# Performance work log

Hardware: AMD Instinct MI355X
Metric: run time of the kernel (lower is better)

## Reference

```python
import jax, jax.numpy as jnp
import numpy as np

B, T, DIM, H, BUCKET = 4, 4096, 1024, 16, 64
E = DIM // H          # head dim = 64
U = T // BUCKET       # number of buckets = 64
EPS = 1e-6


def setup_inputs() -> dict:
    key = jax.random.key(0)
    ks = jax.random.split(key, 5)
    scale = 1.0 / np.sqrt(DIM)
    return {
        "x": jax.random.normal(ks[0], (B, T, DIM), dtype=jnp.float32),
        "Wq": jax.random.normal(ks[1], (DIM, DIM), dtype=jnp.float32) * scale,
        "Wk": jax.random.normal(ks[2], (DIM, DIM), dtype=jnp.float32) * scale,
        "Wv": jax.random.normal(ks[3], (DIM, DIM), dtype=jnp.float32) * scale,
        "Wo": jax.random.normal(ks[4], (DIM, DIM), dtype=jnp.float32) * scale,
        "bo": jnp.zeros((DIM,), dtype=jnp.float32),
    }


def _causal_linear_attn(q, k, v):
    # q, k, v: [b, h, t, e]; psi(k) = elu(k) + 1; q softmaxed over feature dim
    q = jax.nn.softmax(q, axis=-1)
    k = jax.nn.elu(k) + 1.0
    bucket = lambda x: x.reshape(*x.shape[:-2], U, BUCKET, E)  # [b,h,u,n,e]
    b_q, b_k, b_v = bucket(q), bucket(k), bucket(v)
    # cumulative key sums per bucket: [b,h,u,d]
    b_k_cumsum = jnp.cumsum(b_k.sum(axis=-2), axis=2)
    # per-bucket context then cumulative over buckets: [b,h,u,d,e]
    context = jnp.einsum("bhund,bhune->bhude", b_k, b_v)
    context = jnp.cumsum(context, axis=2)
    context = context / (b_k_cumsum[..., None] + EPS)
    # shift by one bucket (blindspot): bucket u sees context through bucket u-1
    context = jnp.concatenate(
        [jnp.zeros_like(context[:, :, :1]), context[:, :, :-1]], axis=2
    )
    attn = jnp.einsum("bhund,bhude->bhune", b_q, context)
    return attn.reshape(q.shape)  # [b,h,t,e]


def reference(x, Wq, Wk, Wv, Wo, bo):
    b, t, _ = x.shape
    q = x @ Wq
    k = x @ Wk
    v = x @ Wv
    merge = lambda z: z.reshape(b, t, H, E).transpose(0, 2, 1, 3)  # [b,h,t,e]
    attn = _causal_linear_attn(merge(q), merge(k), merge(v))
    out = attn.transpose(0, 2, 1, 3).reshape(b, t, DIM)
    return out @ Wo + bo
```

## Files before the change

### kernel.cpp

```cpp
#include <hip/hip_runtime.h>


#define T_LEN 4096
#define DIMN  1024
#define NHEAD 16
#define NB    4
#define MROWS (NB * T_LEN)

typedef float f32x4 __attribute__((ext_vector_type(4)));
typedef short s16x8 __attribute__((ext_vector_type(8)));
typedef short s16x4 __attribute__((ext_vector_type(4)));
using u16 = unsigned short;

__device__ __forceinline__ u16 f2bf(float f) {
  unsigned int u = __float_as_uint(f);
  u += 0x7fffu + ((u >> 16) & 1u);
  return (u16)(u >> 16);
}
__device__ __forceinline__ float bf2f(u16 h) {
  return __uint_as_float(((unsigned int)h) << 16);
}
__device__ __forceinline__ int swz16k(int off) {
  return off ^ (((off >> 7) & 3) << 4);
}

__global__ __launch_bounds__(256) void cvt_all_kern(const float* __restrict__ x,
                                                    const float* __restrict__ W0,
                                                    const float* __restrict__ W1,
                                                    const float* __restrict__ W2,
                                                    const float* __restrict__ W3,
                                                    u16* __restrict__ WT,
                                                    u16* __restrict__ xb) {
  __shared__ float tile[64][65];
  const int tid = threadIdx.x;
  if (blockIdx.x < 1024) {
    const int blk = blockIdx.x & 255;
    const int sel = blockIdx.x >> 8;
    const float* W = (sel == 0) ? W0 : (sel == 1) ? W1 : (sel == 2) ? W2 : W3;
    u16* dst = WT + (size_t)sel * DIMN * DIMN;
    const int k0 = (blk >> 4) << 6;
    const int n0 = (blk & 15) << 6;
    const int r = tid >> 6;
    const int c = tid & 63;
#pragma unroll
    for (int i = 0; i < 16; ++i) {
      int row = (i << 2) + r;
      tile[row][c] = W[(size_t)(k0 + row) * DIMN + n0 + c];
    }
    __syncthreads();
#pragma unroll
    for (int i = 0; i < 16; ++i) {
      int row = (i << 2) + r;
      dst[(size_t)(n0 + row) * DIMN + k0 + c] = f2bf(tile[c][row]);
    }
  } else {
    size_t i = ((size_t)(blockIdx.x - 1024) * 256 + tid) * 4;
    f32x4 v = *(const f32x4*)(x + i);
    s16x4 o;
    o.x = (short)f2bf(v.x); o.y = (short)f2bf(v.y);
    o.z = (short)f2bf(v.z); o.w = (short)f2bf(v.w);
    *(s16x4*)(xb + i) = o;
  }
}

template <int MODE>
__global__ __launch_bounds__(512, 2) void gemm256(
    const u16* __restrict__ A, const u16* __restrict__ Bt,
    u16* __restrict__ dq, u16* __restrict__ dk, u16* __restrict__ dv,
    float* __restrict__ dO, const float* __restrict__ bias) {
  constexpr int K = 1024;
  constexpr int BNT = (MODE == 0) ? 12 : 4;
  constexpr int NT = K / 64;
  extern __shared__ char lds[];

  const int tid = threadIdx.x;
  const int l = tid & 63;
  const int w = tid >> 6;
  const int wm = w >> 2;
  const int wn = w & 3;

  const int xcd = (int)blockIdx.x & 7;
  const int idx = (int)blockIdx.x >> 3;
  const int g = idx / (4 * BNT);
  const int r2 = idx % (4 * BNT);
  const int bn = r2 >> 2;
  const int bm = xcd * 8 + g * 4 + (r2 & 3);
  const size_t arow0 = (size_t)bm * 256;
  const size_t brow0 = (size_t)bn * 256;

  int lrow[2], lcol[2];
#pragma unroll
  for (int i = 0; i < 2; ++i) {
    int lg = swz16k(tid * 16 + i * 8192);
    lrow[i] = lg >> 6;
    lcol[i] = (lg & 63) >> 1;
  }

  const int fr = l & 15;
  const int kswz = (((l >> 4) << 4)) ^ ((((fr >> 1) & 3)) << 4);

  auto STAGE = [&](int matsel, int kh, int tt) {
    const int kbase = (tt & (NT - 1)) * 64 + kh * 32;
#pragma unroll
    for (int i = 0; i < 2; ++i) {
      const u16* src = (matsel == 0)
          ? A  + (arow0 + (size_t)lrow[i]) * K + kbase + lcol[i]
          : Bt + (brow0 + (size_t)lrow[i]) * K + kbase + lcol[i];
      char* dst = lds + ((tt & 1) * 65536 + (matsel * 2 + kh) * 16384 +
                         i * 8192 + w * 1024);
      __builtin_amdgcn_global_load_lds(
          (__attribute__((address_space(1))) const void*)src,
          (__attribute__((address_space(3))) void*)dst, 16, 0, 0);
    }
  };
  auto LDA = [&](int buf, int kh, int rowb) -> s16x8 {
    return *(const s16x8*)(lds + buf * 65536 + kh * 16384 + rowb * 64 + kswz);
  };
  auto LDB = [&](int buf, int kh, int rowb) -> s16x8 {
    return *(const s16x8*)(lds + buf * 65536 + 32768 + kh * 16384 + rowb * 64 + kswz);
  };

  f32x4 acc[8][4];
#pragma unroll
  for (int i = 0; i < 8; ++i)
#pragma unroll
    for (int j = 0; j < 4; ++j) acc[i][j] = {0.f, 0.f, 0.f, 0.f};

  STAGE(0, 0, 0); STAGE(1, 0, 0); STAGE(0, 1, 0); STAGE(1, 1, 0);
  STAGE(0, 0, 1); STAGE(1, 0, 1);
  asm volatile("s_waitcnt vmcnt(8)" ::: "memory");
  __builtin_amdgcn_sched_barrier(0);
  __builtin_amdgcn_s_barrier();

  const int amb = wm * 128;
  const int bnb = wn * 64;
  s16x8 afA[4], afB[4], bfA[4], bfB[4];

#pragma unroll
  for (int i = 0; i < 4; ++i) afA[i] = LDA(0, 0, amb + i * 16 + fr);
#pragma unroll
  for (int i = 0; i < 4; ++i) bfA[i] = LDB(0, 0, bnb + i * 16 + fr);

#define MFMA_BLK(ACCOFF, AF, BF)                                              \
  __builtin_amdgcn_s_setprio(1);                                              \
  _Pragma("unroll")                                                           \
  for (int mi = 0; mi < 4; ++mi)                                              \
    _Pragma("unroll")                                                         \
    for (int ni = 0; ni < 4; ++ni)                                            \
      acc[(ACCOFF) + mi][ni] = __builtin_amdgcn_mfma_f32_16x16x32_bf16(       \
          AF[mi], BF[ni], acc[(ACCOFF) + mi][ni], 0, 0, 0);                   \
  __builtin_amdgcn_s_setprio(0);

#define PHASES(BUF, T)                                                        \
  {                                                                           \
    const int buf = (BUF);                                                    \
    const int t = (T);                                                        \
     \
    STAGE(0, 1, t + 1);                                                       \
    _Pragma("unroll")                                                         \
    for (int i = 0; i < 4; ++i) afB[i] = LDA(buf, 0, amb + (4 + i) * 16 + fr);\
    MFMA_BLK(0, afA, bfA)                                                     \
    __builtin_amdgcn_s_barrier();                                             \
      \
    STAGE(1, 1, t + 1);                                                       \
    asm volatile("s_waitcnt vmcnt(8)" ::: "memory");                          \
    __builtin_amdgcn_sched_barrier(0);                                        \
    _Pragma("unroll")                                                         \
    for (int i = 0; i < 4; ++i) afA[i] = LDA(buf, 1, amb + i * 16 + fr);      \
    _Pragma("unroll")                                                         \
    for (int i = 0; i < 4; ++i) bfB[i] = LDB(buf, 1, bnb + i * 16 + fr);      \
    MFMA_BLK(4, afB, bfA)                                                     \
    __builtin_amdgcn_s_barrier();                                             \
     \
    STAGE(0, 0, t + 2);                                                       \
    _Pragma("unroll")                                                         \
    for (int i = 0; i < 4; ++i) afB[i] = LDA(buf, 1, amb + (4 + i) * 16 + fr);\
    MFMA_BLK(0, afA, bfB)                                                     \
    __builtin_amdgcn_s_barrier();                                             \
       \
    STAGE(1, 0, t + 2);                                                       \
    asm volatile("s_waitcnt vmcnt(8)" ::: "memory");                          \
    __builtin_amdgcn_sched_barrier(0);                                        \
    _Pragma("unroll")                                                         \
    for (int i = 0; i < 4; ++i) afA[i] = LDA(buf ^ 1, 0, amb + i * 16 + fr);  \
    _Pragma("unroll")                                                         \
    for (int i = 0; i < 4; ++i) bfA[i] = LDB(buf ^ 1, 0, bnb + i * 16 + fr);  \
    MFMA_BLK(4, afB, bfB)                                                     \
    __builtin_amdgcn_s_barrier();                                             \
  }

#pragma unroll 1
  for (int th = 0; th < NT / 2; ++th) {
    PHASES(0, 2 * th)
    PHASES(1, 2 * th + 1)
  }
#undef PHASES
#undef MFMA_BLK

  const int r0 = (l >> 4) << 2;
  const int c0 = l & 15;
  if constexpr (MODE == 0) {
    const int mat = bn >> 2;
    u16* dst = (mat == 0) ? dq : ((mat == 1) ? dk : dv);
    const size_t colbase = (size_t)(bn & 3) * 256 + (size_t)wn * 64;
    if (mat == 0) {
#pragma unroll
      for (int mi = 0; mi < 8; ++mi) {
#pragma unroll
        for (int j = 0; j < 4; ++j) {
          float v0 = acc[mi][0][j], v1 = acc[mi][1][j];
          float v2 = acc[mi][2][j], v3 = acc[mi][3][j];
          float m = fmaxf(fmaxf(v0, v1), fmaxf(v2, v3));
#pragma unroll
          for (int off = 1; off < 16; off <<= 1) m = fmaxf(m, __shfl_xor(m, off));
          float e0 = __expf(v0 - m), e1 = __expf(v1 - m);
          float e2 = __expf(v2 - m), e3 = __expf(v3 - m);
          float s = e0 + e1 + e2 + e3;
#pragma unroll
          for (int off = 1; off < 16; off <<= 1) s += __shfl_xor(s, off);
          float inv = 1.f / s;
          const size_t row = arow0 + wm * 128 + mi * 16 + r0 + j;
          u16* p = dst + row * DIMN + colbase + c0;
          p[0]  = f2bf(e0 * inv); p[16] = f2bf(e1 * inv);
          p[32] = f2bf(e2 * inv); p[48] = f2bf(e3 * inv);
        }
      }
    } else {
#pragma unroll
      for (int mi = 0; mi < 8; ++mi)
#pragma unroll
        for (int ni = 0; ni < 4; ++ni)
#pragma unroll
          for (int j = 0; j < 4; ++j) {
            const size_t row = arow0 + wm * 128 + mi * 16 + r0 + j;
            float v = acc[mi][ni][j];
            float r = (mat == 1) ? (v > 0.f ? v + 1.f : __expf(v)) : v;
            dst[row * DIMN + colbase + ni * 16 + c0] = f2bf(r);
          }
    }
  } else {
    asm volatile("s_waitcnt vmcnt(0)" ::: "memory");
    __builtin_amdgcn_sched_barrier(0);
    __builtin_amdgcn_s_barrier();
    float* lf = (float*)lds;
#pragma unroll
    for (int half = 0; half < 2; ++half) {
      if (wm == half) {
#pragma unroll
        for (int mi = 0; mi < 8; ++mi)
#pragma unroll
          for (int ni = 0; ni < 4; ++ni) {
            const int col = wn * 64 + ni * 16 + c0;
            const float bv = bias[brow0 + col];
#pragma unroll
            for (int j = 0; j < 4; ++j) {
              const int row = mi * 16 + r0 + j;
              lf[row * 256 + (col ^ (((row >> 2) & 1) << 4))] =
                  acc[mi][ni][j] + bv;
            }
          }
      }
      __builtin_amdgcn_s_barrier();
#pragma unroll
      for (int i = 0; i < 16; ++i) {
        const int cid = tid + i * 512;
        const int r = cid >> 6;
        const int g2 = (cid & 63) * 4;
        const int pc = g2 ^ (((r >> 2) & 1) << 4);
        f32x4 vv = *(const f32x4*)&lf[r * 256 + pc];
        *(f32x4*)&dO[(arow0 + half * 128 + r) * DIMN + brow0 + g2] = vv;
      }
      __builtin_amdgcn_s_barrier();
    }
  }
}

__global__ __launch_bounds__(256) void ctx_bucket_kern(const u16* __restrict__ kb,
                                                       const u16* __restrict__ vb,
                                                       u16* __restrict__ ctx,
                                                       float* __restrict__ ksum) {
  __shared__ float kl[4096];
  __shared__ float vl[4096];
  const int blk = blockIdx.x;
  const int u = blk & 63;
  const int bh = blk >> 6;
  const int b = bh >> 4, h = bh & 15;
  const size_t rowbase = (size_t)b * T_LEN + (size_t)u * 64;
  const int tid = threadIdx.x;
#pragma unroll
  for (int i = 0; i < 16; ++i) {
    int idx = i * 256 + tid;
    int n = idx >> 6, d = idx & 63;
    size_t g = (rowbase + n) * DIMN + (size_t)h * 64 + d;
    kl[idx] = bf2f(kb[g]);
    vl[idx] = bf2f(vb[g]);
  }
  __syncthreads();
  const int dq = (tid & 15) << 2;
  const int eq = (tid >> 4) << 2;
  float a[4][4] = {};
  float ks[4] = {};
  for (int n = 0; n < 64; ++n) {
    f32x4 kv = *(const f32x4*)&kl[n * 64 + dq];
    f32x4 vv = *(const f32x4*)&vl[n * 64 + eq];
#pragma unroll
    for (int i = 0; i < 4; ++i) {
      ks[i] += kv[i];
#pragma unroll
      for (int j = 0; j < 4; ++j) a[i][j] += kv[i] * vv[j];
    }
  }
  const size_t cbase = (size_t)blk * 4096;
#pragma unroll
  for (int i = 0; i < 4; ++i) {
    s16x4 o;
    o.x = (short)f2bf(a[i][0]); o.y = (short)f2bf(a[i][1]);
    o.z = (short)f2bf(a[i][2]); o.w = (short)f2bf(a[i][3]);
    *(s16x4*)&ctx[cbase + (size_t)(dq + i) * 64 + eq] = o;
  }
  if ((tid >> 4) == 0) {
    f32x4 o = {ks[0], ks[1], ks[2], ks[3]};
    *(f32x4*)&ksum[(size_t)blk * 64 + dq] = o;
  }
}

__global__ __launch_bounds__(256) void ctx_cumnorm_kern(u16* __restrict__ ctx,
                                                        const float* __restrict__ ksum) {
  const int tid = blockIdx.x * 256 + threadIdx.x;
  const int bh = tid >> 10;
  const int rem = tid & 1023;
  const int d = rem >> 4;
  const int e0 = (rem & 15) << 2;
  float c0 = 0.f, c1 = 0.f, c2 = 0.f, c3 = 0.f, accK = 0.f;
  for (int u = 0; u < 64; ++u) {
    const size_t base = ((size_t)(bh * 64 + u)) * 4096 + (size_t)d * 64 + e0;
    s16x4 cv4 = *(const s16x4*)&ctx[base];
    float kk = ksum[(size_t)(bh * 64 + u) * 64 + d];
    float x0 = bf2f((u16)cv4.x), x1 = bf2f((u16)cv4.y);
    float x2 = bf2f((u16)cv4.z), x3 = bf2f((u16)cv4.w);
    s16x4 o;
    if (u == 0) {
      o.x = 0; o.y = 0; o.z = 0; o.w = 0;
    } else {
      float inv = 1.f / (accK + 1e-6f);
      o.x = (short)f2bf(c0 * inv); o.y = (short)f2bf(c1 * inv);
      o.z = (short)f2bf(c2 * inv); o.w = (short)f2bf(c3 * inv);
    }
    *(s16x4*)&ctx[base] = o;
    c0 += x0; c1 += x1; c2 += x2; c3 += x3;
    accK += kk;
  }
}

__global__ __launch_bounds__(256) void attn_bucket_kern(const u16* __restrict__ qb,
                                                        const u16* __restrict__ ctx,
                                                        u16* __restrict__ attn) {
  __shared__ float qT[64 * 68];
  __shared__ float cl[4096];
  const int blk = blockIdx.x;
  const int u = blk & 63;
  const int bh = blk >> 6;
  const int b = bh >> 4, h = bh & 15;
  const size_t rowbase = (size_t)b * T_LEN + (size_t)u * 64;
  const int tid = threadIdx.x;
  const size_t cbase = (size_t)blk * 4096;
#pragma unroll
  for (int i = 0; i < 16; ++i) {
    int idx = i * 256 + tid;
    int n = idx >> 6, d = idx & 63;
    qT[d * 68 + n] = bf2f(qb[(rowbase + n) * DIMN + (size_t)h * 64 + d]);
  }
#pragma unroll
  for (int i = 0; i < 4; ++i) {
    int idx4 = (i * 256 + tid) * 4;
    s16x4 cv = *(const s16x4*)&ctx[cbase + idx4];
    cl[idx4]     = bf2f((u16)cv.x);
    cl[idx4 + 1] = bf2f((u16)cv.y);
    cl[idx4 + 2] = bf2f((u16)cv.z);
    cl[idx4 + 3] = bf2f((u16)cv.w);
  }
  __syncthreads();
  const int nq = (tid & 15) << 2;
  const int eq = (tid >> 4) << 2;
  float a[4][4] = {};
  for (int d = 0; d < 64; ++d) {
    f32x4 qv = *(const f32x4*)&qT[d * 68 + nq];
    f32x4 cv = *(const f32x4*)&cl[d * 64 + eq];
#pragma unroll
    for (int i = 0; i < 4; ++i)
#pragma unroll
      for (int j = 0; j < 4; ++j) a[i][j] += qv[i] * cv[j];
  }
#pragma unroll
  for (int i = 0; i < 4; ++i) {
    s16x4 o;
    o.x = (short)f2bf(a[i][0]); o.y = (short)f2bf(a[i][1]);
    o.z = (short)f2bf(a[i][2]); o.w = (short)f2bf(a[i][3]);
    *(s16x4*)&attn[(rowbase + nq + i) * DIMN + (size_t)h * 64 + eq] = o;
  }
}

extern "C" void kernel_launch(void* const* d_in, const int* in_sizes, int n_in,
                              void* d_out, int out_size, void* d_ws, size_t ws_size,
                              hipStream_t stream) {
  const float* x  = (const float*)d_in[0];
  const float* Wq = (const float*)d_in[1];
  const float* Wk = (const float*)d_in[2];
  const float* Wv = (const float*)d_in[3];
  const float* Wo = (const float*)d_in[4];
  const float* bo = (const float*)d_in[5];
  float* out = (float*)d_out;

  constexpr size_t SZ_XB = (size_t)MROWS * DIMN * 2;
  constexpr size_t SZ_WT = (size_t)DIMN * DIMN * 2;
  constexpr size_t SZ_CTX = (size_t)NB * NHEAD * 64 * 64 * 64 * 2;
  char* ws = (char*)d_ws;
  u16*   xb   = (u16*)(ws);
  u16*   wqT  = (u16*)(ws + SZ_XB);
  u16*   woT  = (u16*)(ws + SZ_XB + 3 * SZ_WT);
  u16*   qb   = (u16*)(ws + SZ_XB + 4 * SZ_WT);
  u16*   kb   = (u16*)(ws + 2 * SZ_XB + 4 * SZ_WT);
  u16*   vb   = (u16*)(ws + 3 * SZ_XB + 4 * SZ_WT);
  u16*   ctx  = (u16*)(ws + 4 * SZ_XB + 4 * SZ_WT);
  float* ksum = (float*)(ws + 4 * SZ_XB + 4 * SZ_WT + SZ_CTX);
  u16*   attn = xb;

  (void)hipFuncSetAttribute((const void*)gemm256<0>,
                            hipFuncAttributeMaxDynamicSharedMemorySize, 131072);
  (void)hipFuncSetAttribute((const void*)gemm256<1>,
                            hipFuncAttributeMaxDynamicSharedMemorySize, 131072);

  cvt_all_kern<<<1024 + MROWS * DIMN / 1024, 256, 0, stream>>>(x, Wq, Wk, Wv, Wo,
                                                               wqT, xb);

  gemm256<0><<<768, 512, 131072, stream>>>(xb, wqT, qb, kb, vb, nullptr, nullptr);

  ctx_bucket_kern<<<NB * NHEAD * 64, 256, 0, stream>>>(kb, vb, ctx, ksum);
  ctx_cumnorm_kern<<<256, 256, 0, stream>>>(ctx, ksum);
  attn_bucket_kern<<<NB * NHEAD * 64, 256, 0, stream>>>(qb, ctx, attn);

  gemm256<1><<<256, 512, 131072, stream>>>(attn, woT, nullptr, nullptr, nullptr, out, bo);
}
```

Measured before the change: 263.9 us.

## Shrink GEMM tiles to 128x256 with K=32 double-buffered stages for higher occupancy

Replaces the 256x256 tile, 64-wide K, four-phase software-pipelined GEMM with a 128x256 tile and 32-wide K step. It uses a simple double-buffer that waits on all outstanding loads each step, 48KB static LDS and launch bounds allowing 4 blocks per CU. Grids double to keep coverage. The output projection epilogue now stores directly to global instead of staging through LDS for coalesced vector stores. The aim is more occupancy and parallel blocks, but it gives up data reuse per tile, finer-grained overlap and coalesced fp32 writes, and adds more barriers.

```diff
diff --git a/kernel.cpp b/kernel.cpp
--- a/kernel.cpp
+++ b/kernel.cpp
@@ -64,14 +64,14 @@
 }
 
 template <int MODE>
-__global__ __launch_bounds__(512, 2) void gemm256(
+__global__ __launch_bounds__(512, 4) void gemm_t(
     const u16* __restrict__ A, const u16* __restrict__ Bt,
     u16* __restrict__ dq, u16* __restrict__ dk, u16* __restrict__ dv,
     float* __restrict__ dO, const float* __restrict__ bias) {
   constexpr int K = 1024;
   constexpr int BNT = (MODE == 0) ? 12 : 4;
-  constexpr int NT = K / 64;
-  extern __shared__ char lds[];
+  constexpr int NT = K / 32;
+  __shared__ char lds[49152];
 
   const int tid = threadIdx.x;
   const int l = tid & 63;
@@ -84,8 +84,8 @@
   const int g = idx / (4 * BNT);
   const int r2 = idx % (4 * BNT);
   const int bn = r2 >> 2;
-  const int bm = xcd * 8 + g * 4 + (r2 & 3);
-  const size_t arow0 = (size_t)bm * 256;
+  const int bm = xcd * 16 + g * 4 + (r2 & 3);
+  const size_t arow0 = (size_t)bm * 128;
   const size_t brow0 = (size_t)bn * 256;
 
   int lrow[2], lcol[2];
@@ -99,103 +99,69 @@
   const int fr = l & 15;
   const int kswz = (((l >> 4) << 4)) ^ ((((fr >> 1) & 3)) << 4);
 
-  auto STAGE = [&](int matsel, int kh, int tt) {
-    const int kbase = (tt & (NT - 1)) * 64 + kh * 32;
+  auto STAGE = [&](int matsel, int tt) {
+    const int kbase = (tt & (NT - 1)) * 32;
 #pragma unroll
     for (int i = 0; i < 2; ++i) {
+      if (matsel == 0 && i == 1) break;
       const u16* src = (matsel == 0)
           ? A  + (arow0 + (size_t)lrow[i]) * K + kbase + lcol[i]
           : Bt + (brow0 + (size_t)lrow[i]) * K + kbase + lcol[i];
-      char* dst = lds + ((tt & 1) * 65536 + (matsel * 2 + kh) * 16384 +
-                         i * 8192 + w * 1024);
+      char* dst = lds + ((tt & 1) * 24576 + matsel * 8192 + i * 8192 + tid * 16);
       __builtin_amdgcn_global_load_lds(
           (__attribute__((address_space(1))) const void*)src,
           (__attribute__((address_space(3))) void*)dst, 16, 0, 0);
     }
   };
-  auto LDA = [&](int buf, int kh, int rowb) -> s16x8 {
-    return *(const s16x8*)(lds + buf * 65536 + kh * 16384 + rowb * 64 + kswz);
+  auto LDA = [&](int buf, int rowb) -> s16x8 {
+    return *(const s16x8*)(lds + buf * 24576 + rowb * 64 + kswz);
   };
-  auto LDB = [&](int buf, int kh, int rowb) -> s16x8 {
-    return *(const s16x8*)(lds + buf * 65536 + 32768 + kh * 16384 + rowb * 64 + kswz);
+  auto LDB = [&](int buf, int rowb) -> s16x8 {
+    return *(const s16x8*)(lds + buf * 24576 + 8192 + rowb * 64 + kswz);
   };
 
-  f32x4 acc[8][4];
-#pragma unroll
-  for (int i = 0; i < 8; ++i)
+  f32x4 acc[4][4];
+#pragma unroll
+  for (int i = 0; i < 4; ++i)
 #pragma unroll
     for (int j = 0; j < 4; ++j) acc[i][j] = {0.f, 0.f, 0.f, 0.f};
 
-  STAGE(0, 0, 0); STAGE(1, 0, 0); STAGE(0, 1, 0); STAGE(1, 1, 0);
-  STAGE(0, 0, 1); STAGE(1, 0, 1);
-  asm volatile("s_waitcnt vmcnt(8)" ::: "memory");
+  STAGE(0, 0); STAGE(1, 0);
+  asm volatile("s_waitcnt vmcnt(0)" ::: "memory");
   __builtin_amdgcn_sched_barrier(0);
   __builtin_amdgcn_s_barrier();
 
-  const int amb = wm * 128;
+  const int amb = wm * 64;
   const int bnb = wn * 64;
-  s16x8 afA[4], afB[4], bfA[4], bfB[4];
-
-#pragma unroll
-  for (int i = 0; i < 4; ++i) afA[i] = LDA(0, 0, amb + i * 16 + fr);
-#pragma unroll
-  for (int i = 0; i < 4; ++i) bfA[i] = LDB(0, 0, bnb + i * 16 + fr);
-
-#define MFMA_BLK(ACCOFF, AF, BF)                                              \
-  __builtin_amdgcn_s_setprio(1);                                              \
-  _Pragma("unroll")                                                           \
-  for (int mi = 0; mi < 4; ++mi)                                              \
+  s16x8 af[4], bf[4];
+
+#define STEP(BUF, T)                                                          \
+  {                                                                           \
+    STAGE(0, (T) + 1);                                                        \
+    STAGE(1, (T) + 1);                                                        \
     _Pragma("unroll")                                                         \
-    for (int ni = 0; ni < 4; ++ni)                                            \
-      acc[(ACCOFF) + mi][ni] = __builtin_amdgcn_mfma_f32_16x16x32_bf16(       \
-          AF[mi], BF[ni], acc[(ACCOFF) + mi][ni], 0, 0, 0);                   \
-  __builtin_amdgcn_s_setprio(0);
-
-#define PHASES(BUF, T)                                                        \
-  {                                                                           \
-    const int buf = (BUF);                                                    \
-    const int t = (T);                                                        \
-     \
-    STAGE(0, 1, t + 1);                                                       \
+    for (int i = 0; i < 4; ++i) af[i] = LDA((BUF), amb + i * 16 + fr);        \
     _Pragma("unroll")                                                         \
-    for (int i = 0; i < 4; ++i) afB[i] = LDA(buf, 0, amb + (4 + i) * 16 + fr);\
-    MFMA_BLK(0, afA, bfA)                                                     \
-    __builtin_amdgcn_s_barrier();                                             \
-      \
-    STAGE(1, 1, t + 1);                                                       \
-    asm volatile("s_waitcnt vmcnt(8)" ::: "memory");                          \
+    for (int i = 0; i < 4; ++i) bf[i] = LDB((BUF), bnb + i * 16 + fr);        \
+    __builtin_amdgcn_s_setprio(1);                                            \
+    _Pragma("unroll")                                                         \
+    for (int mi = 0; mi < 4; ++mi)                                            \
+      _Pragma("unroll")                                                       \
+      for (int ni = 0; ni < 4; ++ni)                                          \
+        acc[mi][ni] = __builtin_amdgcn_mfma_f32_16x16x32_bf16(                \
+            af[mi], bf[ni], acc[mi][ni], 0, 0, 0);                            \
+    __builtin_amdgcn_s_setprio(0);                                            \
+    asm volatile("s_waitcnt vmcnt(0)" ::: "memory");                          \
     __builtin_amdgcn_sched_barrier(0);                                        \
-    _Pragma("unroll")                                                         \
-    for (int i = 0; i < 4; ++i) afA[i] = LDA(buf, 1, amb + i * 16 + fr);      \
-    _Pragma("unroll")                                                         \
-    for (int i = 0; i < 4; ++i) bfB[i] = LDB(buf, 1, bnb + i * 16 + fr);      \
-    MFMA_BLK(4, afB, bfA)                                                     \
-    __builtin_amdgcn_s_barrier();                                             \
-     \
-    STAGE(0, 0, t + 2);                                                       \
-    _Pragma("unroll")                                                         \
-    for (int i = 0; i < 4; ++i) afB[i] = LDA(buf, 1, amb + (4 + i) * 16 + fr);\
-    MFMA_BLK(0, afA, bfB)                                                     \
-    __builtin_amdgcn_s_barrier();                                             \
-       \
-    STAGE(1, 0, t + 2);                                                       \
-    asm volatile("s_waitcnt vmcnt(8)" ::: "memory");                          \
-    __builtin_amdgcn_sched_barrier(0);                                        \
-    _Pragma("unroll")                                                         \
-    for (int i = 0; i < 4; ++i) afA[i] = LDA(buf ^ 1, 0, amb + i * 16 + fr);  \
-    _Pragma("unroll")                                                         \
-    for (int i = 0; i < 4; ++i) bfA[i] = LDB(buf ^ 1, 0, bnb + i * 16 + fr);  \
-    MFMA_BLK(4, afB, bfB)                                                     \
     __builtin_amdgcn_s_barrier();                                             \
   }
 
 #pragma unroll 1
   for (int th = 0; th < NT / 2; ++th) {
-    PHASES(0, 2 * th)
-    PHASES(1, 2 * th + 1)
-  }
-#undef PHASES
-#undef MFMA_BLK
+    STEP(0, 2 * th)
+    STEP(1, 2 * th + 1)
+  }
+#undef STEP
 
   const int r0 = (l >> 4) << 2;
   const int c0 = l & 15;
@@ -205,7 +171,7 @@
     const size_t colbase = (size_t)(bn & 3) * 256 + (size_t)wn * 64;
     if (mat == 0) {
 #pragma unroll
-      for (int mi = 0; mi < 8; ++mi) {
+      for (int mi = 0; mi < 4; ++mi) {
 #pragma unroll
         for (int j = 0; j < 4; ++j) {
           float v0 = acc[mi][0][j], v1 = acc[mi][1][j];
@@ -219,7 +185,7 @@
 #pragma unroll
           for (int off = 1; off < 16; off <<= 1) s += __shfl_xor(s, off);
           float inv = 1.f / s;
-          const size_t row = arow0 + wm * 128 + mi * 16 + r0 + j;
+          const size_t row = arow0 + wm * 64 + mi * 16 + r0 + j;
           u16* p = dst + row * DIMN + colbase + c0;
           p[0]  = f2bf(e0 * inv); p[16] = f2bf(e1 * inv);
           p[32] = f2bf(e2 * inv); p[48] = f2bf(e3 * inv);
@@ -227,51 +193,30 @@
       }
     } else {
 #pragma unroll
-      for (int mi = 0; mi < 8; ++mi)
+      for (int mi = 0; mi < 4; ++mi)
 #pragma unroll
         for (int ni = 0; ni < 4; ++ni)
 #pragma unroll
           for (int j = 0; j < 4; ++j) {
-            const size_t row = arow0 + wm * 128 + mi * 16 + r0 + j;
+            const size_t row = arow0 + wm * 64 + mi * 16 + r0 + j;
             float v = acc[mi][ni][j];
             float r = (mat == 1) ? (v > 0.f ? v + 1.f : __expf(v)) : v;
             dst[row * DIMN + colbase + ni * 16 + c0] = f2bf(r);
           }
     }
   } else {
-    asm volatile("s_waitcnt vmcnt(0)" ::: "memory");
-    __builtin_amdgcn_sched_barrier(0);
-    __builtin_amdgcn_s_barrier();
-    float* lf = (float*)lds;
-#pragma unroll
-    for (int half = 0; half < 2; ++half) {
-      if (wm == half) {
-#pragma unroll
-        for (int mi = 0; mi < 8; ++mi)
-#pragma unroll
-          for (int ni = 0; ni < 4; ++ni) {
-            const int col = wn * 64 + ni * 16 + c0;
-            const float bv = bias[brow0 + col];
-#pragma unroll
-            for (int j = 0; j < 4; ++j) {
-              const int row = mi * 16 + r0 + j;
-              lf[row * 256 + (col ^ (((row >> 2) & 1) << 4))] =
-                  acc[mi][ni][j] + bv;
-            }
-          }
+#pragma unroll
+    for (int mi = 0; mi < 4; ++mi)
+#pragma unroll
+      for (int ni = 0; ni < 4; ++ni) {
+        const size_t col = brow0 + (size_t)wn * 64 + ni * 16 + c0;
+        const float bv = bias[col];
+#pragma unroll
+        for (int j = 0; j < 4; ++j) {
+          const size_t row = arow0 + wm * 64 + mi * 16 + r0 + j;
+          dO[row * DIMN + col] = acc[mi][ni][j] + bv;
+        }
       }
-      __builtin_amdgcn_s_barrier();
-#pragma unroll
-      for (int i = 0; i < 16; ++i) {
-        const int cid = tid + i * 512;
-        const int r = cid >> 6;
-        const int g2 = (cid & 63) * 4;
-        const int pc = g2 ^ (((r >> 2) & 1) << 4);
-        f32x4 vv = *(const f32x4*)&lf[r * 256 + pc];
-        *(f32x4*)&dO[(arow0 + half * 128 + r) * DIMN + brow0 + g2] = vv;
-      }
-      __builtin_amdgcn_s_barrier();
-    }
   }
 }
 
@@ -425,19 +370,14 @@
   float* ksum = (float*)(ws + 4 * SZ_XB + 4 * SZ_WT + SZ_CTX);
   u16*   attn = xb;
 
-  (void)hipFuncSetAttribute((const void*)gemm256<0>,
-                            hipFuncAttributeMaxDynamicSharedMemorySize, 131072);
-  (void)hipFuncSetAttribute((const void*)gemm256<1>,
-                            hipFuncAttributeMaxDynamicSharedMemorySize, 131072);
-
   cvt_all_kern<<<1024 + MROWS * DIMN / 1024, 256, 0, stream>>>(x, Wq, Wk, Wv, Wo,
                                                                wqT, xb);
 
-  gemm256<0><<<768, 512, 131072, stream>>>(xb, wqT, qb, kb, vb, nullptr, nullptr);
+  gemm_t<0><<<1536, 512, 0, stream>>>(xb, wqT, qb, kb, vb, nullptr, nullptr);
 
   ctx_bucket_kern<<<NB * NHEAD * 64, 256, 0, stream>>>(kb, vb, ctx, ksum);
   ctx_cumnorm_kern<<<256, 256, 0, stream>>>(ctx, ksum);
   attn_bucket_kern<<<NB * NHEAD * 64, 256, 0, stream>>>(qb, ctx, attn);
 
-  gemm256<1><<<256, 512, 131072, stream>>>(attn, woT, nullptr, nullptr, nullptr, out, bo);
-}
+  gemm_t<1><<<512, 512, 0, stream>>>(attn, woT, nullptr, nullptr, nullptr, out, bo);
+}
```

Result: no change. 262.8 us (-0.4%).
